# Optimization experiments

Measured on AMD Instinct MI355X. Metric: run time of the kernel, lower is better.

The kernel has to match this reference:

```python
import jax, jax.numpy as jnp
import numpy as np

N = 50000
E = 300000
D_IN = 256
D_OUT = 256


def setup_inputs() -> dict:
    key = jax.random.key(0)
    ks = jax.random.split(key, 9)
    obj_vecs = jax.random.normal(ks[0], (N, D_IN), dtype=jnp.float32)
    rel_vecs = jax.random.normal(ks[1], (N, D_IN), dtype=jnp.float32)
    edge_index = jax.random.randint(ks[2], (E, 2), 0, N, dtype=jnp.int64)
    s = 1.0 / np.sqrt(D_IN)
    # SAGEConv params: lin_l (applied to aggregated neighbors, with bias),
    # lin_r (applied to root/self features, no bias). One pair per conv.
    W_l_obj = jax.random.uniform(ks[3], (D_OUT, D_IN), minval=-s, maxval=s, dtype=jnp.float32)
    b_l_obj = jax.random.uniform(ks[4], (D_OUT,), minval=-s, maxval=s, dtype=jnp.float32)
    W_r_obj = jax.random.uniform(ks[5], (D_OUT, D_IN), minval=-s, maxval=s, dtype=jnp.float32)
    W_l_rel = jax.random.uniform(ks[6], (D_OUT, D_IN), minval=-s, maxval=s, dtype=jnp.float32)
    b_l_rel = jax.random.uniform(ks[7], (D_OUT,), minval=-s, maxval=s, dtype=jnp.float32)
    W_r_rel = jax.random.uniform(ks[8], (D_OUT, D_IN), minval=-s, maxval=s, dtype=jnp.float32)
    return {"obj_vecs": obj_vecs, "rel_vecs": rel_vecs, "edge_index": edge_index,
            "W_l_obj": W_l_obj, "b_l_obj": b_l_obj, "W_r_obj": W_r_obj,
            "W_l_rel": W_l_rel, "b_l_rel": b_l_rel, "W_r_rel": W_r_rel}


def _sage_conv(x, src, dst, W_l, b_l, W_r):
    # mean aggregation of source-node features at destination nodes
    msg = x[src]                                             # [E, D_IN] gather
    summed = jax.ops.segment_sum(msg, dst, num_segments=N)   # [N, D_IN]
    cnt = jax.ops.segment_sum(jnp.ones((src.shape[0],), x.dtype), dst, num_segments=N)
    agg = summed / jnp.maximum(cnt, 1.0)[:, None]
    # out = lin_l(agg) + lin_r(x)
    return agg @ W_l.T + b_l + x @ W_r.T


def reference(obj_vecs, rel_vecs, edge_index,
              W_l_obj, b_l_obj, W_r_obj, W_l_rel, b_l_rel, W_r_rel):
    # module transposes [E,2] -> [2,E]; PyG: messages flow src=row0 -> dst=row1
    src = edge_index[:, 0]
    dst = edge_index[:, 1]
    obj_out = _sage_conv(obj_vecs, src, dst, W_l_obj, b_l_obj, W_r_obj)
    rel_out = _sage_conv(rel_vecs, src, dst, W_l_rel, b_l_rel, W_r_rel)
    return (obj_out, rel_out)
```

## Files before the change

### kernel.cpp

```cpp
#include <hip/hip_runtime.h>

#define N_NODES 50000
#define N_EDGES 300000
#define DFEAT 256
#define KCAT 512
#define MT 32
#define APAD 8
#define AROW (KCAT + APAD)
#define SCAN_NBLK ((N_NODES + 255) / 256)

typedef __attribute__((ext_vector_type(8))) short bf16x8;
typedef __attribute__((ext_vector_type(4))) float f32x4;

__device__ __forceinline__ unsigned short f2bf(float f) {
    union { float f; unsigned int u; } c; c.f = f;
    unsigned int r = c.u + 0x7FFF + ((c.u >> 16) & 1);
    return (unsigned short)(r >> 16);
}

__global__ void k_zero(int4* __restrict__ p, int n4) {
    int i = blockIdx.x * blockDim.x + threadIdx.x;
    int stride = gridDim.x * blockDim.x;
    for (; i < n4; i += stride) p[i] = make_int4(0, 0, 0, 0);
}

__global__ void k_hist(const int* __restrict__ ei, int* __restrict__ cnt, int E) {
    int e = blockIdx.x * blockDim.x + threadIdx.x;
    if (e < E) {
        unsigned d = (unsigned)ei[2 * e + 1];
        if (d < (unsigned)N_NODES) atomicAdd(&cnt[d], 1);
    }
}

__global__ void k_scan_a(const int* __restrict__ cnt, int* __restrict__ bsum, int n) {
    int b = blockIdx.x, t = threadIdx.x;
    int i = b * 256 + t;
    int v = (i < n) ? cnt[i] : 0;
    #pragma unroll
    for (int d = 32; d; d >>= 1) v += __shfl_down(v, d, 64);
    __shared__ int ws[4];
    if ((t & 63) == 0) ws[t >> 6] = v;
    __syncthreads();
    if (t == 0) bsum[b] = ws[0] + ws[1] + ws[2] + ws[3];
}

__global__ void k_scan_b(const int* __restrict__ bsum, int* __restrict__ bpre,
                         int* __restrict__ off, int nblk, int n) {
    __shared__ int lds[256];
    int t = threadIdx.x;
    int v = (t < nblk) ? bsum[t] : 0;
    lds[t] = v;
    __syncthreads();
    for (int d = 1; d < 256; d <<= 1) {
        int u = (t >= d) ? lds[t - d] : 0;
        __syncthreads();
        lds[t] += u;
        __syncthreads();
    }
    if (t < nblk) bpre[t] = lds[t] - v;
    if (t == 255) off[n] = lds[255];
}

__global__ void k_scan_c(const int* __restrict__ cnt, const int* __restrict__ bpre,
                         int* __restrict__ off, int* __restrict__ cursor, int n) {
    __shared__ int lds[256];
    int b = blockIdx.x, t = threadIdx.x;
    int i = b * 256 + t;
    int v = (i < n) ? cnt[i] : 0;
    lds[t] = v;
    __syncthreads();
    for (int d = 1; d < 256; d <<= 1) {
        int u = (t >= d) ? lds[t - d] : 0;
        __syncthreads();
        lds[t] += u;
        __syncthreads();
    }
    if (i < n) {
        int ex = bpre[b] + lds[t] - v;
        off[i] = ex;
        cursor[i] = ex;
    }
}

__global__ void k_scatter(const int* __restrict__ ei, int* __restrict__ cursor,
                          int* __restrict__ srcs, int E) {
    int e = blockIdx.x * blockDim.x + threadIdx.x;
    if (e < E) {
        unsigned s = (unsigned)ei[2 * e];
        unsigned d = (unsigned)ei[2 * e + 1];
        if (d < (unsigned)N_NODES && s < (unsigned)N_NODES) {
            unsigned pos = (unsigned)atomicAdd(&cursor[d], 1);
            if (pos < (unsigned)E) srcs[pos] = (int)s;
        }
    }
}

__global__ void k_wt(const float* __restrict__ Wl, const float* __restrict__ Wr,
                     unsigned short* __restrict__ Wb) {
    int id = blockIdx.x * blockDim.x + threadIdx.x;
    int j    = id & 7;
    int lane = (id >> 3) & 63;
    int frag = id >> 9;
    int nt   = frag & 15;
    int kb   = frag >> 4;
    int k = kb * 32 + (lane >> 4) * 8 + j;
    int n = nt * 16 + (lane & 15);
    float v = (k < 256) ? Wl[n * 256 + k] : Wr[n * 256 + (k - 256)];
    Wb[id] = f2bf(v);
}

__global__ __launch_bounds__(256, 4)
void k_fused(const float* __restrict__ x_obj, const float* __restrict__ x_rel,
             const unsigned short* __restrict__ Wb_obj, const unsigned short* __restrict__ Wb_rel,
             const float* __restrict__ b_obj, const float* __restrict__ b_rel,
             const int* __restrict__ off, const int* __restrict__ srcs,
             float* __restrict__ out, int n) {
    __shared__ unsigned short A[MT][AROW];

    const int tz = blockIdx.y;
    const float* __restrict__ x   = tz ? x_rel  : x_obj;
    const unsigned short* __restrict__ Wb = tz ? Wb_rel : Wb_obj;
    const float* __restrict__ bia = tz ? b_rel  : b_obj;
    float* __restrict__ outp = out + (size_t)tz * (size_t)N_NODES * DFEAT;

    const int t = threadIdx.x;
    const int wave = t >> 6, lane = t & 63;
    const int node0 = blockIdx.x * MT;

    const float4* __restrict__ x4 = (const float4*)x;
    for (int il = wave; il < MT; il += 4) {
        int node = node0 + il;
        float4 accv = make_float4(0.f, 0.f, 0.f, 0.f);
        float4 xv   = make_float4(0.f, 0.f, 0.f, 0.f);
        if (node < n) {
            xv = x4[(size_t)node * 64 + lane];
            int eb = off[node], ee = off[node + 1];
            if (eb < 0) eb = 0;
            if (ee > N_EDGES) ee = N_EDGES;
            if (ee < eb) ee = eb;
            int e = eb;
            for (; e + 3 < ee; e += 4) {
                unsigned s0 = (unsigned)srcs[e],     s1 = (unsigned)srcs[e + 1];
                unsigned s2 = (unsigned)srcs[e + 2], s3 = (unsigned)srcs[e + 3];
                if (s0 >= (unsigned)n) s0 = 0;
                if (s1 >= (unsigned)n) s1 = 0;
                if (s2 >= (unsigned)n) s2 = 0;
                if (s3 >= (unsigned)n) s3 = 0;
                float4 v0 = x4[(size_t)s0 * 64 + lane];
                float4 v1 = x4[(size_t)s1 * 64 + lane];
                float4 v2 = x4[(size_t)s2 * 64 + lane];
                float4 v3 = x4[(size_t)s3 * 64 + lane];
                accv.x += (v0.x + v1.x) + (v2.x + v3.x);
                accv.y += (v0.y + v1.y) + (v2.y + v3.y);
                accv.z += (v0.z + v1.z) + (v2.z + v3.z);
                accv.w += (v0.w + v1.w) + (v2.w + v3.w);
            }
            if (e + 1 < ee) {
                unsigned s0 = (unsigned)srcs[e], s1 = (unsigned)srcs[e + 1];
                if (s0 >= (unsigned)n) s0 = 0;
                if (s1 >= (unsigned)n) s1 = 0;
                float4 v0 = x4[(size_t)s0 * 64 + lane];
                float4 v1 = x4[(size_t)s1 * 64 + lane];
                accv.x += v0.x + v1.x; accv.y += v0.y + v1.y;
                accv.z += v0.z + v1.z; accv.w += v0.w + v1.w;
                e += 2;
            }
            if (e < ee) {
                unsigned s0 = (unsigned)srcs[e];
                if (s0 >= (unsigned)n) s0 = 0;
                float4 v = x4[(size_t)s0 * 64 + lane];
                accv.x += v.x; accv.y += v.y; accv.z += v.z; accv.w += v.w;
            }
            float c = (float)(ee - eb);
            float inv = 1.0f / fmaxf(c, 1.0f);
            accv.x *= inv; accv.y *= inv; accv.z *= inv; accv.w *= inv;
        }
        ushort4 a16 = make_ushort4(f2bf(accv.x), f2bf(accv.y), f2bf(accv.z), f2bf(accv.w));
        ushort4 x16 = make_ushort4(f2bf(xv.x),  f2bf(xv.y),  f2bf(xv.z),  f2bf(xv.w));
        *(ushort4*)&A[il][4 * lane]       = a16;
        *(ushort4*)&A[il][256 + 4 * lane] = x16;
    }
    __syncthreads();

    const int r0  = (wave & 1) * 16;
    const int nt0 = (wave >> 1) * 8;
    const int lq  = lane >> 4;
    const int lm  = lane & 15;

    f32x4 acc[8];
    #pragma unroll
    for (int ct = 0; ct < 8; ct++) {
        float b = bia[(nt0 + ct) * 16 + lm];
        acc[ct] = (f32x4){b, b, b, b};
    }

    const bf16x8* __restrict__ Wb8 = (const bf16x8*)Wb;
    #pragma unroll
    for (int kb = 0; kb < 16; kb++) {
        bf16x8 af = *(const bf16x8*)&A[r0 + lm][kb * 32 + lq * 8];
        #pragma unroll
        for (int ct = 0; ct < 8; ct++) {
            bf16x8 bf = Wb8[(size_t)(kb * 16 + nt0 + ct) * 64 + lane];
            acc[ct] = __builtin_amdgcn_mfma_f32_16x16x32_bf16(af, bf, acc[ct], 0, 0, 0);
        }
    }

    #pragma unroll
    for (int ct = 0; ct < 8; ct++) {
        int col = (nt0 + ct) * 16 + lm;
        #pragma unroll
        for (int r = 0; r < 4; r++) {
            int node = node0 + r0 + lq * 4 + r;
            if (node < n) outp[((size_t)node << 8) + col] = acc[ct][r];
        }
    }
}

extern "C" void kernel_launch(void* const* d_in, const int* in_sizes, int n_in,
                              void* d_out, int out_size, void* d_ws, size_t ws_size,
                              hipStream_t stream) {
    const float* obj  = (const float*)d_in[0];
    const float* rel  = (const float*)d_in[1];
    const int*   ei   = (const int*)d_in[2];
    const float* Wl_o = (const float*)d_in[3];
    const float* bl_o = (const float*)d_in[4];
    const float* Wr_o = (const float*)d_in[5];
    const float* Wl_r = (const float*)d_in[6];
    const float* bl_r = (const float*)d_in[7];
    const float* Wr_r = (const float*)d_in[8];
    float* out = (float*)d_out;

    char* w = (char*)d_ws;
    size_t o = 0;
    auto alloc = [&](size_t b) { size_t r = o; o += (b + 255) & ~(size_t)255; return r; };
    size_t csr_base = o;
    int*            cnt    = (int*)(w + alloc((size_t)N_NODES * 4));
    int*            off    = (int*)(w + alloc((size_t)(N_NODES + 1) * 4));
    int*            cursor = (int*)(w + alloc((size_t)N_NODES * 4));
    int*            srcs   = (int*)(w + alloc((size_t)N_EDGES * 4));
    size_t csr_bytes = o - csr_base;
    int*            bsum   = (int*)(w + alloc(256 * 4));
    int*            bpre   = (int*)(w + alloc(256 * 4));
    unsigned short* Wb_o   = (unsigned short*)(w + alloc((size_t)KCAT * DFEAT * 2));
    unsigned short* Wb_r   = (unsigned short*)(w + alloc((size_t)KCAT * DFEAT * 2));

    int n4 = (int)(csr_bytes / 16);
    k_zero<<<512, 256, 0, stream>>>((int4*)(w + csr_base), n4);
    k_hist<<<(N_EDGES + 255) / 256, 256, 0, stream>>>(ei, cnt, N_EDGES);
    k_scan_a<<<SCAN_NBLK, 256, 0, stream>>>(cnt, bsum, N_NODES);
    k_scan_b<<<1, 256, 0, stream>>>(bsum, bpre, off, SCAN_NBLK, N_NODES);
    k_scan_c<<<SCAN_NBLK, 256, 0, stream>>>(cnt, bpre, off, cursor, N_NODES);
    k_scatter<<<(N_EDGES + 255) / 256, 256, 0, stream>>>(ei, cursor, srcs, N_EDGES);
    k_wt<<<(KCAT * DFEAT) / 256, 256, 0, stream>>>(Wl_o, Wr_o, Wb_o);
    k_wt<<<(KCAT * DFEAT) / 256, 256, 0, stream>>>(Wl_r, Wr_r, Wb_r);

    dim3 g((N_NODES + MT - 1) / MT, 2);
    k_fused<<<g, 256, 0, stream>>>(obj, rel, Wb_o, Wb_r, bl_o, bl_r, off, srcs, out, N_NODES);
}
```

Measured before the change: 352.2 us.

## Collapse CSR build into fewer kernels and halve fused tile height

Merges weight conversion and counter zeroing into one prep kernel. The three-pass scan is replaced by a single kernel where each wave does a wave-level scan and claims its base offset with an atomic, so the CSR segments are no longer in node order. The fused kernel now reads per-node counts instead of off[node+1], uses 16-node tiles with 4 column tiles per wave, and raises the launch-bounds occupancy hint. The goal is to cut launch count and serial scan latency and to raise occupancy in the gather, at the cost of less locality in the srcs array and more reloads of the weight fragments across tiles.

```diff
diff --git a/kernel.cpp b/kernel.cpp
--- a/kernel.cpp
+++ b/kernel.cpp
@@ -4,10 +4,10 @@
 #define N_EDGES 300000
 #define DFEAT 256
 #define KCAT 512
-#define MT 32
+#define MT 16
 #define APAD 8
 #define AROW (KCAT + APAD)
-#define SCAN_NBLK ((N_NODES + 255) / 256)
+#define NWELEM (KCAT * DFEAT)
 
 typedef __attribute__((ext_vector_type(8))) short bf16x8;
 typedef __attribute__((ext_vector_type(4))) float f32x4;
@@ -18,102 +18,77 @@
     return (unsigned short)(r >> 16);
 }
 
-__global__ void k_zero(int4* __restrict__ p, int n4) {
-    int i = blockIdx.x * blockDim.x + threadIdx.x;
-    int stride = gridDim.x * blockDim.x;
-    for (; i < n4; i += stride) p[i] = make_int4(0, 0, 0, 0);
-}
-
-__global__ void k_hist(const int* __restrict__ ei, int* __restrict__ cnt, int E) {
-    int e = blockIdx.x * blockDim.x + threadIdx.x;
-    if (e < E) {
-        unsigned d = (unsigned)ei[2 * e + 1];
-        if (d < (unsigned)N_NODES) atomicAdd(&cnt[d], 1);
-    }
-}
-
-__global__ void k_scan_a(const int* __restrict__ cnt, int* __restrict__ bsum, int n) {
-    int b = blockIdx.x, t = threadIdx.x;
-    int i = b * 256 + t;
-    int v = (i < n) ? cnt[i] : 0;
-    #pragma unroll
-    for (int d = 32; d; d >>= 1) v += __shfl_down(v, d, 64);
-    __shared__ int ws[4];
-    if ((t & 63) == 0) ws[t >> 6] = v;
-    __syncthreads();
-    if (t == 0) bsum[b] = ws[0] + ws[1] + ws[2] + ws[3];
-}
-
-__global__ void k_scan_b(const int* __restrict__ bsum, int* __restrict__ bpre,
-                         int* __restrict__ off, int nblk, int n) {
-    __shared__ int lds[256];
-    int t = threadIdx.x;
-    int v = (t < nblk) ? bsum[t] : 0;
-    lds[t] = v;
-    __syncthreads();
-    for (int d = 1; d < 256; d <<= 1) {
-        int u = (t >= d) ? lds[t - d] : 0;
-        __syncthreads();
-        lds[t] += u;
-        __syncthreads();
-    }
-    if (t < nblk) bpre[t] = lds[t] - v;
-    if (t == 255) off[n] = lds[255];
-}
-
-__global__ void k_scan_c(const int* __restrict__ cnt, const int* __restrict__ bpre,
-                         int* __restrict__ off, int* __restrict__ cursor, int n) {
-    __shared__ int lds[256];
-    int b = blockIdx.x, t = threadIdx.x;
-    int i = b * 256 + t;
-    int v = (i < n) ? cnt[i] : 0;
-    lds[t] = v;
-    __syncthreads();
-    for (int d = 1; d < 256; d <<= 1) {
-        int u = (t >= d) ? lds[t - d] : 0;
-        __syncthreads();
-        lds[t] += u;
-        __syncthreads();
-    }
-    if (i < n) {
-        int ex = bpre[b] + lds[t] - v;
-        off[i] = ex;
-        cursor[i] = ex;
-    }
-}
-
-__global__ void k_scatter(const int* __restrict__ ei, int* __restrict__ cursor,
-                          int* __restrict__ srcs, int E) {
-    int e = blockIdx.x * blockDim.x + threadIdx.x;
-    if (e < E) {
-        unsigned s = (unsigned)ei[2 * e];
-        unsigned d = (unsigned)ei[2 * e + 1];
-        if (d < (unsigned)N_NODES && s < (unsigned)N_NODES) {
-            unsigned pos = (unsigned)atomicAdd(&cursor[d], 1);
-            if (pos < (unsigned)E) srcs[pos] = (int)s;
-        }
-    }
-}
-
-__global__ void k_wt(const float* __restrict__ Wl, const float* __restrict__ Wr,
-                     unsigned short* __restrict__ Wb) {
+__global__ void k_prep(const float* __restrict__ Wl_o, const float* __restrict__ Wr_o,
+                       const float* __restrict__ Wl_r, const float* __restrict__ Wr_r,
+                       unsigned short* __restrict__ Wb_o, unsigned short* __restrict__ Wb_r,
+                       int* __restrict__ cnt, int* __restrict__ total) {
     int id = blockIdx.x * blockDim.x + threadIdx.x;
-    int j    = id & 7;
-    int lane = (id >> 3) & 63;
-    int frag = id >> 9;
+    int wid  = id & (NWELEM - 1);
+    int j    = wid & 7;
+    int lane = (wid >> 3) & 63;
+    int frag = wid >> 9;
     int nt   = frag & 15;
     int kb   = frag >> 4;
     int k = kb * 32 + (lane >> 4) * 8 + j;
     int n = nt * 16 + (lane & 15);
-    float v = (k < 256) ? Wl[n * 256 + k] : Wr[n * 256 + (k - 256)];
-    Wb[id] = f2bf(v);
-}
-
-__global__ __launch_bounds__(256, 4)
+    if (id < NWELEM) {
+        float v = (k < 256) ? Wl_o[n * 256 + k] : Wr_o[n * 256 + (k - 256)];
+        Wb_o[wid] = f2bf(v);
+    } else {
+        float v = (k < 256) ? Wl_r[n * 256 + k] : Wr_r[n * 256 + (k - 256)];
+        Wb_r[wid] = f2bf(v);
+    }
+    if (id < N_NODES) cnt[id] = 0;
+    if (id == 0) *total = 0;
+}
+
+__global__ void k_hist(const int2* __restrict__ ei, int* __restrict__ cnt, int E) {
+    int e = blockIdx.x * blockDim.x + threadIdx.x;
+    if (e < E) {
+        unsigned d = (unsigned)ei[e].y;
+        if (d < (unsigned)N_NODES) atomicAdd(&cnt[d], 1);
+    }
+}
+
+__global__ void k_alloc(const int* __restrict__ cnt, int* __restrict__ off,
+                        int* __restrict__ cursor, int* __restrict__ total, int n) {
+    int i = blockIdx.x * blockDim.x + threadIdx.x;
+    int lane = threadIdx.x & 63;
+    int v = (i < n) ? cnt[i] : 0;
+    int s = v;
+    #pragma unroll
+    for (int d = 1; d < 64; d <<= 1) {
+        int u = __shfl_up(s, d, 64);
+        if (lane >= d) s += u;
+    }
+    int wsum = __shfl(s, 63, 64);
+    int base = 0;
+    if (lane == 63) base = atomicAdd(total, wsum);
+    base = __shfl(base, 63, 64);
+    int ex = base + s - v;
+    if (i < n) { off[i] = ex; cursor[i] = ex; }
+}
+
+__global__ void k_scatter(const int2* __restrict__ ei, int* __restrict__ cursor,
+                          int* __restrict__ srcs, int E) {
+    int e = blockIdx.x * blockDim.x + threadIdx.x;
+    if (e < E) {
+        int2 sd = ei[e];
+        unsigned s = (unsigned)sd.x;
+        unsigned d = (unsigned)sd.y;
+        if (d < (unsigned)N_NODES) {
+            unsigned pos = (unsigned)atomicAdd(&cursor[d], 1);
+            if (pos < (unsigned)E) srcs[pos] = (s < (unsigned)N_NODES) ? (int)s : 0;
+        }
+    }
+}
+
+__global__ __launch_bounds__(256, 8)
 void k_fused(const float* __restrict__ x_obj, const float* __restrict__ x_rel,
              const unsigned short* __restrict__ Wb_obj, const unsigned short* __restrict__ Wb_rel,
              const float* __restrict__ b_obj, const float* __restrict__ b_rel,
-             const int* __restrict__ off, const int* __restrict__ srcs,
+             const int* __restrict__ off, const int* __restrict__ cnt,
+             const int* __restrict__ srcs,
              float* __restrict__ out, int n) {
     __shared__ unsigned short A[MT][AROW];
 
@@ -134,8 +109,11 @@
         float4 xv   = make_float4(0.f, 0.f, 0.f, 0.f);
         if (node < n) {
             xv = x4[(size_t)node * 64 + lane];
-            int eb = off[node], ee = off[node + 1];
+            int eb = off[node];
+            int ec = cnt[node];
             if (eb < 0) eb = 0;
+            if (ec < 0) ec = 0;
+            int ee = eb + ec;
             if (ee > N_EDGES) ee = N_EDGES;
             if (ee < eb) ee = eb;
             int e = eb;
@@ -182,14 +160,13 @@
     }
     __syncthreads();
 
-    const int r0  = (wave & 1) * 16;
-    const int nt0 = (wave >> 1) * 8;
+    const int nt0 = wave * 4;
     const int lq  = lane >> 4;
     const int lm  = lane & 15;
 
-    f32x4 acc[8];
-    #pragma unroll
-    for (int ct = 0; ct < 8; ct++) {
+    f32x4 acc[4];
+    #pragma unroll
+    for (int ct = 0; ct < 4; ct++) {
         float b = bia[(nt0 + ct) * 16 + lm];
         acc[ct] = (f32x4){b, b, b, b};
     }
@@ -197,20 +174,20 @@
     const bf16x8* __restrict__ Wb8 = (const bf16x8*)Wb;
     #pragma unroll
     for (int kb = 0; kb < 16; kb++) {
-        bf16x8 af = *(const bf16x8*)&A[r0 + lm][kb * 32 + lq * 8];
+        bf16x8 af = *(const bf16x8*)&A[lm][kb * 32 + lq * 8];
         #pragma unroll
-        for (int ct = 0; ct < 8; ct++) {
+        for (int ct = 0; ct < 4; ct++) {
             bf16x8 bf = Wb8[(size_t)(kb * 16 + nt0 + ct) * 64 + lane];
             acc[ct] = __builtin_amdgcn_mfma_f32_16x16x32_bf16(af, bf, acc[ct], 0, 0, 0);
         }
     }
 
     #pragma unroll
-    for (int ct = 0; ct < 8; ct++) {
+    for (int ct = 0; ct < 4; ct++) {
         int col = (nt0 + ct) * 16 + lm;
         #pragma unroll
         for (int r = 0; r < 4; r++) {
-            int node = node0 + r0 + lq * 4 + r;
+            int node = node0 + lq * 4 + r;
             if (node < n) outp[((size_t)node << 8) + col] = acc[ct][r];
         }
     }
@@ -221,7 +198,7 @@
                               hipStream_t stream) {
     const float* obj  = (const float*)d_in[0];
     const float* rel  = (const float*)d_in[1];
-    const int*   ei   = (const int*)d_in[2];
+    const int2*  ei   = (const int2*)d_in[2];
     const float* Wl_o = (const float*)d_in[3];
     const float* bl_o = (const float*)d_in[4];
     const float* Wr_o = (const float*)d_in[5];
@@ -233,27 +210,19 @@
     char* w = (char*)d_ws;
     size_t o = 0;
     auto alloc = [&](size_t b) { size_t r = o; o += (b + 255) & ~(size_t)255; return r; };
-    size_t csr_base = o;
     int*            cnt    = (int*)(w + alloc((size_t)N_NODES * 4));
-    int*            off    = (int*)(w + alloc((size_t)(N_NODES + 1) * 4));
+    int*            off    = (int*)(w + alloc((size_t)N_NODES * 4));
     int*            cursor = (int*)(w + alloc((size_t)N_NODES * 4));
     int*            srcs   = (int*)(w + alloc((size_t)N_EDGES * 4));
-    size_t csr_bytes = o - csr_base;
-    int*            bsum   = (int*)(w + alloc(256 * 4));
-    int*            bpre   = (int*)(w + alloc(256 * 4));
-    unsigned short* Wb_o   = (unsigned short*)(w + alloc((size_t)KCAT * DFEAT * 2));
-    unsigned short* Wb_r   = (unsigned short*)(w + alloc((size_t)KCAT * DFEAT * 2));
-
-    int n4 = (int)(csr_bytes / 16);
-    k_zero<<<512, 256, 0, stream>>>((int4*)(w + csr_base), n4);
+    int*            total  = (int*)(w + alloc(256));
+    unsigned short* Wb_o   = (unsigned short*)(w + alloc((size_t)NWELEM * 2));
+    unsigned short* Wb_r   = (unsigned short*)(w + alloc((size_t)NWELEM * 2));
+
+    k_prep<<<(2 * NWELEM) / 256, 256, 0, stream>>>(Wl_o, Wr_o, Wl_r, Wr_r, Wb_o, Wb_r, cnt, total);
     k_hist<<<(N_EDGES + 255) / 256, 256, 0, stream>>>(ei, cnt, N_EDGES);
-    k_scan_a<<<SCAN_NBLK, 256, 0, stream>>>(cnt, bsum, N_NODES);
-    k_scan_b<<<1, 256, 0, stream>>>(bsum, bpre, off, SCAN_NBLK, N_NODES);
-    k_scan_c<<<SCAN_NBLK, 256, 0, stream>>>(cnt, bpre, off, cursor, N_NODES);
+    k_alloc<<<(N_NODES + 255) / 256, 256, 0, stream>>>(cnt, off, cursor, total, N_NODES);
     k_scatter<<<(N_EDGES + 255) / 256, 256, 0, stream>>>(ei, cursor, srcs, N_EDGES);
-    k_wt<<<(KCAT * DFEAT) / 256, 256, 0, stream>>>(Wl_o, Wr_o, Wb_o);
-    k_wt<<<(KCAT * DFEAT) / 256, 256, 0, stream>>>(Wl_r, Wr_r, Wb_r);
 
     dim3 g((N_NODES + MT - 1) / MT, 2);
-    k_fused<<<g, 256, 0, stream>>>(obj, rel, Wb_o, Wb_r, bl_o, bl_r, off, srcs, out, N_NODES);
-}
+    k_fused<<<g, 256, 0, stream>>>(obj, rel, Wb_o, Wb_r, bl_o, bl_r, off, cnt, srcs, out, N_NODES);
+}
```

After: 331.1 us. -6.0%, faster.
